# Kernel tuning notes

Measured on AMD Instinct MI355X. Metric: run time of the kernel, lower is better.

Reference implementation:

```python
import jax, jax.numpy as jnp
import numpy as np

B, Q, DIM, HEADS, HEAD_DIM, KV = 32, 4, 2048, 16, 128, 8192


def setup_inputs() -> dict:
    key = jax.random.key(0)
    ks = jax.random.split(key, 9)
    s = 0.02
    return {
        'x': jax.random.normal(ks[0], (B, Q, DIM), jnp.float32),
        'attn_bias': jax.random.normal(ks[1], (B, HEADS, Q, KV), jnp.float32),
        'cache_k': jax.random.normal(ks[2], (B, KV, HEAD_DIM), jnp.float32),
        'cache_v': jax.random.normal(ks[3], (B, KV, HEAD_DIM), jnp.float32),
        'wq': jax.random.normal(ks[4], (DIM, HEADS, HEAD_DIM), jnp.float32) * s,
        'bq': jnp.zeros((HEADS, HEAD_DIM), jnp.float32),
        'wk': jax.random.normal(ks[5], (DIM, HEAD_DIM), jnp.float32) * s,
        'bk': jnp.zeros((HEAD_DIM,), jnp.float32),
        'wv': jax.random.normal(ks[6], (DIM, HEAD_DIM), jnp.float32) * s,
        'bv': jnp.zeros((HEAD_DIM,), jnp.float32),
        'wo': jax.random.normal(ks[7], (HEADS, HEAD_DIM, DIM), jnp.float32) * s,
        'bo': jnp.zeros((DIM,), jnp.float32),
    }


def reference(x, attn_bias, cache_k, cache_v, wq, bq, wk, bk, wv, bv, wo, bo):
    q_len = x.shape[1]
    # projections (MQA: shared single-head K/V)
    q = jnp.einsum('bqd,dhe->bqhe', x, wq) + bq          # [B,Q,H,hd]
    k_new = x @ wk + bk                                   # [B,Q,hd]
    v_new = x @ wv + bv
    # rolling KV cache update: shift left by q_len, write new tokens at end
    k = jnp.roll(cache_k, -q_len, axis=1).at[:, -q_len:].set(k_new)  # [B,KV,hd]
    v = jnp.roll(cache_v, -q_len, axis=1).at[:, -q_len:].set(v_new)
    scale = 1.0 / (k.shape[-1] ** 0.5)
    p = jnp.einsum('bqhe,bke->bhqk', q, k) * scale        # [B,H,Q,KV]
    a = jax.nn.softmax(p + attn_bias, axis=-1)
    o = jnp.einsum('bhqk,bke->bqhe', a, v)                # [B,Q,H,hd]
    return jnp.einsum('bqhe,hed->bqd', o, wo) + bo        # [B,Q,DIM]
```

## Files before the change

kernel.cpp:

```cpp
#include <hip/hip_runtime.h>
#include <cstddef>
#include <cstdint>

#define BATCH 32
#define QL 4
#define DIM 2048
#define NH 16
#define HD 128
#define KVLEN 8192
#define HQ 64
#define CHUNK 512
#define NCK 16
#define KT 64
#define NT 8

typedef __attribute__((ext_vector_type(8))) short bf16x8;
typedef __attribute__((ext_vector_type(4))) float f32x4;

__device__ __forceinline__ unsigned short cvt_bf16(float f) {
    unsigned int u = __builtin_bit_cast(unsigned int, f);
    u += 0x7fffu + ((u >> 16) & 1u);
    return (unsigned short)(u >> 16);
}
__device__ __forceinline__ unsigned int pack2(float a, float b) {
    return (unsigned int)cvt_bf16(a) | ((unsigned int)cvt_bf16(b) << 16);
}
__device__ __forceinline__ float bf16_to_f32(unsigned short s) {
    unsigned int u = ((unsigned int)s) << 16;
    return __builtin_bit_cast(float, u);
}
__device__ __forceinline__ bf16x8 mk_frag(unsigned int a, unsigned int b,
                                          unsigned int c, unsigned int d) {
    unsigned int t[4] = {a, b, c, d};
    return *(const bf16x8*)t;
}

template<int VARIANT>
__global__ __launch_bounds__(256) void gemm_kernel(
    const float* __restrict__ A,
    const float* __restrict__ w0p, const float* __restrict__ w1p,
    const float* __restrict__ w2p,
    const float* __restrict__ b0p, const float* __restrict__ b1p,
    const float* __restrict__ b2p,
    float* __restrict__ o0, float* __restrict__ o1, float* __restrict__ o2)
{
    const int n0 = blockIdx.x * 64;
    const int m0 = blockIdx.y * 64;
    const int kz = blockIdx.z * 512;
    const int tid = threadIdx.x;
    const int wave = tid >> 6, lane = tid & 63;
    const int l15 = lane & 15, quad = lane >> 4;

    const float* W; const float* Bv; int ldw, nc;
    if (VARIANT == 0) {
        if (n0 >= 2176)      { W = w2p; Bv = b2p; ldw = 128;  nc = n0 - 2176; }
        else if (n0 >= 2048) { W = w1p; Bv = b1p; ldw = 128;  nc = n0 - 2048; }
        else                 { W = w0p; Bv = b0p; ldw = 2048; nc = n0; }
    } else { W = w0p; Bv = b0p; ldw = 2048; nc = n0; }

    __shared__ alignas(16) unsigned short a_s[64][72];
    __shared__ alignas(16) unsigned short w_s[64][68];

    const int wn = tid & 63;
    const int wk0 = (tid >> 6) * 4;

    f32x4 acc[4];
    #pragma unroll
    for (int nt = 0; nt < 4; ++nt) acc[nt] = (f32x4){0.f, 0.f, 0.f, 0.f};

    float4 apre[4];
    float wpre[4][4];

    #pragma unroll
    for (int ii = 0; ii < 4; ++ii) {
        int f = tid + 256 * ii, r = f >> 4, c4 = (f & 15) << 2;
        apre[ii] = *(const float4*)&A[(size_t)(m0 + r) * DIM + kz + c4];
    }
    #pragma unroll
    for (int sub = 0; sub < 4; ++sub) {
        int k0 = kz + wk0 + 16 * sub;
        const float* wp = W + (size_t)k0 * ldw + nc + wn;
        #pragma unroll
        for (int j = 0; j < 4; ++j) wpre[sub][j] = wp[(size_t)j * ldw];
    }

    for (int it = 0; it < 8; ++it) {
        __syncthreads();
        #pragma unroll
        for (int ii = 0; ii < 4; ++ii) {
            int f = tid + 256 * ii, r = f >> 4, c4 = (f & 15) << 2;
            *(uint2*)&a_s[r][c4] =
                make_uint2(pack2(apre[ii].x, apre[ii].y), pack2(apre[ii].z, apre[ii].w));
        }
        #pragma unroll
        for (int sub = 0; sub < 4; ++sub) {
            int k0 = wk0 + 16 * sub;
            *(uint2*)&w_s[wn][k0] =
                make_uint2(pack2(wpre[sub][0], wpre[sub][1]),
                           pack2(wpre[sub][2], wpre[sub][3]));
        }
        __syncthreads();
        if (it + 1 < 8) {
            const int kb = kz + (it + 1) * 64;
            #pragma unroll
            for (int ii = 0; ii < 4; ++ii) {
                int f = tid + 256 * ii, r = f >> 4, c4 = (f & 15) << 2;
                apre[ii] = *(const float4*)&A[(size_t)(m0 + r) * DIM + kb + c4];
            }
            #pragma unroll
            for (int sub = 0; sub < 4; ++sub) {
                int k0 = kb + wk0 + 16 * sub;
                const float* wp = W + (size_t)k0 * ldw + nc + wn;
                #pragma unroll
                for (int j = 0; j < 4; ++j) wpre[sub][j] = wp[(size_t)j * ldw];
            }
        }
        #pragma unroll
        for (int kf = 0; kf < 2; ++kf) {
            bf16x8 af = *(const bf16x8*)&a_s[16 * wave + l15][kf * 32 + quad * 8];
            #pragma unroll
            for (int nt = 0; nt < 4; ++nt) {
                uint2 lo = *(const uint2*)&w_s[nt * 16 + l15][kf * 32 + quad * 8];
                uint2 hi = *(const uint2*)&w_s[nt * 16 + l15][kf * 32 + quad * 8 + 4];
                bf16x8 wf = mk_frag(lo.x, lo.y, hi.x, hi.y);
                acc[nt] = __builtin_amdgcn_mfma_f32_16x16x32_bf16(af, wf, acc[nt], 0, 0, 0);
            }
        }
    }
    const bool addb = (blockIdx.z == 0);
    #pragma unroll
    for (int nt = 0; nt < 4; ++nt)
        #pragma unroll
        for (int reg = 0; reg < 4; ++reg) {
            int row = m0 + 16 * wave + quad * 4 + reg;
            int col = n0 + nt * 16 + l15;
            float s = acc[nt][reg];
            if (VARIANT == 1) {
                atomicAdd(&o0[(size_t)row * DIM + col], s + (addb ? Bv[col] : 0.f));
            } else {
                int b = row >> 2, q = row & 3;
                if (col < 2048) {
                    int h = col >> 7, e = col & 127;
                    atomicAdd(&o0[((size_t)(b * 64 + h * 4 + q)) * 128 + e],
                              s + (addb ? b0p[col] : 0.f));
                } else if (col < 2176) {
                    int e = col - 2048;
                    atomicAdd(&o1[(size_t)row * 128 + e], s + (addb ? b1p[e] : 0.f));
                } else {
                    int e = col - 2176;
                    atomicAdd(&o2[(size_t)row * 128 + e], s + (addb ? b2p[e] : 0.f));
                }
            }
        }
}

__global__ __launch_bounds__(256, 2) void attn_kernel(
    const float* __restrict__ qws, const float* __restrict__ kws,
    const float* __restrict__ vws,
    const float* __restrict__ cachek, const float* __restrict__ cachev,
    const float* __restrict__ abias,
    float* __restrict__ opart, float* __restrict__ lpart)
{
    const int ck = blockIdx.x;
    const int b  = blockIdx.y;
    const int tid = threadIdx.x;
    const int wave = tid >> 6, lane = tid & 63;
    const int l15 = lane & 15, quad = lane >> 4;
    const float scale = 0.08838834764831845f;

    __shared__ alignas(16) unsigned short k_s[KT][136];
    __shared__ alignas(16) unsigned short v_sT[HD][68];
    __shared__ alignas(16) unsigned short p_s[4][16][72];

    bf16x8 qf[4];
    {
        const float* qrow = qws + ((size_t)b * HQ + 16 * wave + l15) * HD;
        #pragma unroll
        for (int kf = 0; kf < 4; ++kf) {
            float4 f0 = *(const float4*)&qrow[kf * 32 + quad * 8];
            float4 f1 = *(const float4*)&qrow[kf * 32 + quad * 8 + 4];
            qf[kf] = mk_frag(pack2(f0.x, f0.y), pack2(f0.z, f0.w),
                             pack2(f1.x, f1.y), pack2(f1.z, f1.w));
        }
    }

    const int kbase0 = ck * CHUNK;
    const int ve = tid & 127;
    const int vkq = (tid >> 7);

    const float* bptr[4];
    #pragma unroll
    for (int reg = 0; reg < 4; ++reg) {
        int hq = 16 * wave + quad * 4 + reg;
        int h = hq >> 2, q = hq & 3;
        bptr[reg] = abias + (((size_t)(b * NH + h)) * QL + q) * KVLEN + kbase0 + l15;
    }

    float4 kpre[8];
    float vpre[8][4];
    float bpre[16];

    #pragma unroll
    for (int i = 0; i < 8; ++i) {
        int f = tid + 256 * i;
        int row = f >> 5, e0 = (f & 31) << 2;
        int kv = kbase0 + row;
        const float* pk = (kv < KVLEN - QL)
            ? cachek + ((size_t)b * KVLEN + kv + QL) * HD + e0
            : kws + ((size_t)b * QL + (kv - (KVLEN - QL))) * HD + e0;
        kpre[i] = *(const float4*)pk;
    }
    #pragma unroll
    for (int i = 0; i < 8; ++i) {
        int kv0 = kbase0 + (vkq + 2 * i) * 4;
        #pragma unroll
        for (int j = 0; j < 4; ++j) {
            int kv = kv0 + j;
            const float* pv = (kv < KVLEN - QL)
                ? cachev + ((size_t)b * KVLEN + kv + QL) * HD + ve
                : vws + ((size_t)b * QL + (kv - (KVLEN - QL))) * HD + ve;
            vpre[i][j] = *pv;
        }
    }
    #pragma unroll
    for (int nt = 0; nt < 4; ++nt)
        #pragma unroll
        for (int reg = 0; reg < 4; ++reg)
            bpre[nt * 4 + reg] = bptr[reg][nt * 16];

    f32x4 oa[8];
    #pragma unroll
    for (int n8 = 0; n8 < 8; ++n8) oa[n8] = (f32x4){0.f, 0.f, 0.f, 0.f};
    float lrow[4] = {0.f, 0.f, 0.f, 0.f};

    for (int t = 0; t < NT; ++t) {
        __syncthreads();
        #pragma unroll
        for (int i = 0; i < 8; ++i) {
            int f = tid + 256 * i;
            int row = f >> 5, e0 = (f & 31) << 2;
            *(uint2*)&k_s[row][e0] =
                make_uint2(pack2(kpre[i].x, kpre[i].y), pack2(kpre[i].z, kpre[i].w));
        }
        #pragma unroll
        for (int i = 0; i < 8; ++i) {
            int kv0 = (vkq + 2 * i) * 4;
            *(uint2*)&v_sT[ve][kv0] =
                make_uint2(pack2(vpre[i][0], vpre[i][1]),
                           pack2(vpre[i][2], vpre[i][3]));
        }
        float bias[16];
        #pragma unroll
        for (int j = 0; j < 16; ++j) bias[j] = bpre[j];
        __syncthreads();
        if (t + 1 < NT) {
            const int tb = kbase0 + (t + 1) * KT;
            #pragma unroll
            for (int i = 0; i < 8; ++i) {
                int f = tid + 256 * i;
                int row = f >> 5, e0 = (f & 31) << 2;
                int kv = tb + row;
                const float* pk = (kv < KVLEN - QL)
                    ? cachek + ((size_t)b * KVLEN + kv + QL) * HD + e0
                    : kws + ((size_t)b * QL + (kv - (KVLEN - QL))) * HD + e0;
                kpre[i] = *(const float4*)pk;
            }
            #pragma unroll
            for (int i = 0; i < 8; ++i) {
                int kv0 = tb + (vkq + 2 * i) * 4;
                #pragma unroll
                for (int j = 0; j < 4; ++j) {
                    int kv = kv0 + j;
                    const float* pv = (kv < KVLEN - QL)
                        ? cachev + ((size_t)b * KVLEN + kv + QL) * HD + ve
                        : vws + ((size_t)b * QL + (kv - (KVLEN - QL))) * HD + ve;
                    vpre[i][j] = *pv;
                }
            }
            #pragma unroll
            for (int nt = 0; nt < 4; ++nt)
                #pragma unroll
                for (int reg = 0; reg < 4; ++reg)
                    bpre[nt * 4 + reg] = bptr[reg][(t + 1) * KT + nt * 16];
        }
        f32x4 sacc[4];
        #pragma unroll
        for (int nt = 0; nt < 4; ++nt) sacc[nt] = (f32x4){0.f, 0.f, 0.f, 0.f};
        __builtin_amdgcn_s_setprio(1);
        #pragma unroll
        for (int kf = 0; kf < 4; ++kf) {
            #pragma unroll
            for (int nt = 0; nt < 4; ++nt) {
                bf16x8 kfb = *(const bf16x8*)&k_s[nt * 16 + l15][kf * 32 + quad * 8];
                sacc[nt] = __builtin_amdgcn_mfma_f32_16x16x32_bf16(qf[kf], kfb, sacc[nt], 0, 0, 0);
            }
        }
        __builtin_amdgcn_s_setprio(0);
        #pragma unroll
        for (int nt = 0; nt < 4; ++nt)
            #pragma unroll
            for (int reg = 0; reg < 4; ++reg) {
                float s = sacc[nt][reg] * scale + bias[nt * 4 + reg];
                float p = __expf(s);
                unsigned short pb = cvt_bf16(p);
                lrow[reg] += bf16_to_f32(pb);
                p_s[wave][quad * 4 + reg][nt * 16 + l15] = pb;
            }
        __builtin_amdgcn_s_setprio(1);
        #pragma unroll
        for (int kfp = 0; kfp < 2; ++kfp) {
            uint2 plo = *(const uint2*)&p_s[wave][l15][kfp * 32 + quad * 8];
            uint2 phi = *(const uint2*)&p_s[wave][l15][kfp * 32 + quad * 8 + 4];
            bf16x8 pf = mk_frag(plo.x, plo.y, phi.x, phi.y);
            #pragma unroll
            for (int n8 = 0; n8 < 8; ++n8) {
                uint2 vlo = *(const uint2*)&v_sT[n8 * 16 + l15][kfp * 32 + quad * 8];
                uint2 vhi = *(const uint2*)&v_sT[n8 * 16 + l15][kfp * 32 + quad * 8 + 4];
                bf16x8 vf = mk_frag(vlo.x, vlo.y, vhi.x, vhi.y);
                oa[n8] = __builtin_amdgcn_mfma_f32_16x16x32_bf16(pf, vf, oa[n8], 0, 0, 0);
            }
        }
        __builtin_amdgcn_s_setprio(0);
    }
    #pragma unroll
    for (int reg = 0; reg < 4; ++reg) {
        float v = lrow[reg];
        v += __shfl_xor(v, 1);
        v += __shfl_xor(v, 2);
        v += __shfl_xor(v, 4);
        v += __shfl_xor(v, 8);
        lrow[reg] = v;
    }
    const size_t obase = ((size_t)(b * NCK + ck)) * HQ * HD;
    #pragma unroll
    for (int n8 = 0; n8 < 8; ++n8)
        #pragma unroll
        for (int reg = 0; reg < 4; ++reg) {
            int hq = 16 * wave + quad * 4 + reg;
            int e = n8 * 16 + l15;
            opart[obase + (size_t)hq * HD + e] = oa[n8][reg];
        }
    if (l15 == 0) {
        #pragma unroll
        for (int reg = 0; reg < 4; ++reg) {
            int hq = 16 * wave + quad * 4 + reg;
            lpart[(size_t)(b * NCK + ck) * HQ + hq] = lrow[reg];
        }
    }
}

__global__ __launch_bounds__(128) void combine_kernel(
    const float* __restrict__ opart, const float* __restrict__ lpart,
    float* __restrict__ ored, float* __restrict__ outz)
{
    const int bh = blockIdx.x;
    const int b = bh >> 6, hq = bh & 63;
    const int e = threadIdx.x;
    outz[(size_t)bh * 128 + e] = 0.f;
    float lt = 0.f, ov = 0.f;
    #pragma unroll
    for (int c = 0; c < NCK; ++c) {
        lt += lpart[(b * NCK + c) * HQ + hq];
        ov += opart[((size_t)(b * NCK + c) * HQ + hq) * HD + e];
    }
    int h = hq >> 2, q = hq & 3;
    ored[(size_t)(b * QL + q) * DIM + h * HD + e] = ov / lt;
}

extern "C" void kernel_launch(void* const* d_in, const int* in_sizes, int n_in,
                              void* d_out, int out_size, void* d_ws, size_t ws_size,
                              hipStream_t stream)
{
    const float* x   = (const float*)d_in[0];
    const float* ab  = (const float*)d_in[1];
    const float* cK  = (const float*)d_in[2];
    const float* cV  = (const float*)d_in[3];
    const float* wq  = (const float*)d_in[4];
    const float* bq  = (const float*)d_in[5];
    const float* wk  = (const float*)d_in[6];
    const float* bk  = (const float*)d_in[7];
    const float* wv  = (const float*)d_in[8];
    const float* bv  = (const float*)d_in[9];
    const float* wo  = (const float*)d_in[10];
    const float* bo  = (const float*)d_in[11];
    float* out = (float*)d_out;

    float* ws   = (float*)d_ws;
    float* wsq  = ws;
    float* wsk  = wsq + 262144;
    float* wsv  = wsk + 16384;
    float* wsop = wsv + 16384;
    float* wsl  = wsop + 4194304;
    float* wsor = wsl + 32768;

    hipMemsetAsync(ws, 0, (size_t)(262144 + 16384 + 16384) * sizeof(float),
                   stream);

    gemm_kernel<0><<<dim3(36, 2, 4), 256, 0, stream>>>(
        x, wq, wk, wv, bq, bk, bv, wsq, wsk, wsv);
    attn_kernel<<<dim3(NCK, BATCH), 256, 0, stream>>>(
        wsq, wsk, wsv, cK, cV, ab, wsop, wsl);
    combine_kernel<<<BATCH * HQ, 128, 0, stream>>>(wsop, wsl, wsor, out);
    gemm_kernel<1><<<dim3(32, 2, 4), 256, 0, stream>>>(
        wsor, wo, nullptr, nullptr, bo, nullptr, nullptr, out, nullptr, nullptr);
}
```

Baseline: 397.3 us.

## Remove combine kernel via atomic split-KV accumulation and fused normalization in output GEMM

The attention kernel now accumulates its partial outputs and row sums directly into a per-batch buffer with atomics, instead of writing per-chunk partials that a separate combine kernel reduced. The 1/l normalization and the head-layout transpose move into the A-load of the output-projection GEMM, and zeroing of the output moves into the first GEMM. The KV chunk is halved so the attention grid has twice as many blocks. This removes one kernel launch and the large partial-output round trip through memory, at the cost of atomic contention across chunks and float results that are not bit-for-bit deterministic.

```diff
diff --git a/kernel.cpp b/kernel.cpp
--- a/kernel.cpp
+++ b/kernel.cpp
@@ -9,10 +9,10 @@
 #define HD 128
 #define KVLEN 8192
 #define HQ 64
-#define CHUNK 512
-#define NCK 16
+#define CHUNK 256
+#define NCKB 32
 #define KT 64
-#define NT 8
+#define NT 4
 
 typedef __attribute__((ext_vector_type(8))) short bf16x8;
 typedef __attribute__((ext_vector_type(4))) float f32x4;
@@ -42,7 +42,8 @@
     const float* __restrict__ w2p,
     const float* __restrict__ b0p, const float* __restrict__ b1p,
     const float* __restrict__ b2p,
-    float* __restrict__ o0, float* __restrict__ o1, float* __restrict__ o2)
+    float* __restrict__ o0, float* __restrict__ o1, float* __restrict__ o2,
+    float* __restrict__ zout)
 {
     const int n0 = blockIdx.x * 64;
     const int m0 = blockIdx.y * 64;
@@ -51,12 +52,23 @@
     const int wave = tid >> 6, lane = tid & 63;
     const int l15 = lane & 15, quad = lane >> 4;
 
+    if (VARIANT == 0) {
+        int gbid = (blockIdx.z * 2 + blockIdx.y) * 36 + blockIdx.x;
+        int base = gbid * 256 + tid;
+        #pragma unroll
+        for (int i = 0; i < 4; ++i) {
+            int idx = base + 73728 * i;
+            if (idx < 262144) zout[idx] = 0.f;
+        }
+    }
+
     const float* W; const float* Bv; int ldw, nc;
     if (VARIANT == 0) {
         if (n0 >= 2176)      { W = w2p; Bv = b2p; ldw = 128;  nc = n0 - 2176; }
         else if (n0 >= 2048) { W = w1p; Bv = b1p; ldw = 128;  nc = n0 - 2048; }
         else                 { W = w0p; Bv = b0p; ldw = 2048; nc = n0; }
     } else { W = w0p; Bv = b0p; ldw = 2048; nc = n0; }
+    const float* Lp = w1p;
 
     __shared__ alignas(16) unsigned short a_s[64][72];
     __shared__ alignas(16) unsigned short w_s[64][68];
@@ -74,7 +86,16 @@
     #pragma unroll
     for (int ii = 0; ii < 4; ++ii) {
         int f = tid + 256 * ii, r = f >> 4, c4 = (f & 15) << 2;
-        apre[ii] = *(const float4*)&A[(size_t)(m0 + r) * DIM + kz + c4];
+        int row = m0 + r, cc = kz + c4;
+        if (VARIANT == 1) {
+            int bb = row >> 2, q = row & 3, h = cc >> 7, e0 = cc & 127;
+            int hq = h * 4 + q;
+            float4 v = *(const float4*)&A[((size_t)(bb * 64 + hq)) * 128 + e0];
+            float linv = 1.0f / Lp[bb * 64 + hq];
+            apre[ii] = make_float4(v.x * linv, v.y * linv, v.z * linv, v.w * linv);
+        } else {
+            apre[ii] = *(const float4*)&A[(size_t)row * DIM + cc];
+        }
     }
     #pragma unroll
     for (int sub = 0; sub < 4; ++sub) {
@@ -105,7 +126,16 @@
             #pragma unroll
             for (int ii = 0; ii < 4; ++ii) {
                 int f = tid + 256 * ii, r = f >> 4, c4 = (f & 15) << 2;
-                apre[ii] = *(const float4*)&A[(size_t)(m0 + r) * DIM + kb + c4];
+                int row = m0 + r, cc = kb + c4;
+                if (VARIANT == 1) {
+                    int bb = row >> 2, q = row & 3, h = cc >> 7, e0 = cc & 127;
+                    int hq = h * 4 + q;
+                    float4 v = *(const float4*)&A[((size_t)(bb * 64 + hq)) * 128 + e0];
+                    float linv = 1.0f / Lp[bb * 64 + hq];
+                    apre[ii] = make_float4(v.x * linv, v.y * linv, v.z * linv, v.w * linv);
+                } else {
+                    apre[ii] = *(const float4*)&A[(size_t)row * DIM + cc];
+                }
             }
             #pragma unroll
             for (int sub = 0; sub < 4; ++sub) {
@@ -159,7 +189,7 @@
     const float* __restrict__ vws,
     const float* __restrict__ cachek, const float* __restrict__ cachev,
     const float* __restrict__ abias,
-    float* __restrict__ opart, float* __restrict__ lpart)
+    float* __restrict__ oacc, float* __restrict__ lacc)
 {
     const int ck = blockIdx.x;
     const int b  = blockIdx.y;
@@ -331,40 +361,22 @@
         v += __shfl_xor(v, 8);
         lrow[reg] = v;
     }
-    const size_t obase = ((size_t)(b * NCK + ck)) * HQ * HD;
+    const size_t abase = (size_t)b * HQ * HD;
     #pragma unroll
     for (int n8 = 0; n8 < 8; ++n8)
         #pragma unroll
         for (int reg = 0; reg < 4; ++reg) {
             int hq = 16 * wave + quad * 4 + reg;
             int e = n8 * 16 + l15;
-            opart[obase + (size_t)hq * HD + e] = oa[n8][reg];
+            atomicAdd(&oacc[abase + (size_t)hq * HD + e], oa[n8][reg]);
         }
     if (l15 == 0) {
         #pragma unroll
         for (int reg = 0; reg < 4; ++reg) {
             int hq = 16 * wave + quad * 4 + reg;
-            lpart[(size_t)(b * NCK + ck) * HQ + hq] = lrow[reg];
-        }
-    }
-}
-
-__global__ __launch_bounds__(128) void combine_kernel(
-    const float* __restrict__ opart, const float* __restrict__ lpart,
-    float* __restrict__ ored, float* __restrict__ outz)
-{
-    const int bh = blockIdx.x;
-    const int b = bh >> 6, hq = bh & 63;
-    const int e = threadIdx.x;
-    outz[(size_t)bh * 128 + e] = 0.f;
-    float lt = 0.f, ov = 0.f;
-    #pragma unroll
-    for (int c = 0; c < NCK; ++c) {
-        lt += lpart[(b * NCK + c) * HQ + hq];
-        ov += opart[((size_t)(b * NCK + c) * HQ + hq) * HD + e];
-    }
-    int h = hq >> 2, q = hq & 3;
-    ored[(size_t)(b * QL + q) * DIM + h * HD + e] = ov / lt;
+            atomicAdd(&lacc[b * HQ + hq], lrow[reg]);
+        }
+    }
 }
 
 extern "C" void kernel_launch(void* const* d_in, const int* in_sizes, int n_in,
@@ -389,18 +401,18 @@
     float* wsq  = ws;
     float* wsk  = wsq + 262144;
     float* wsv  = wsk + 16384;
-    float* wsop = wsv + 16384;
-    float* wsl  = wsop + 4194304;
-    float* wsor = wsl + 32768;
-
-    hipMemsetAsync(ws, 0, (size_t)(262144 + 16384 + 16384) * sizeof(float),
-                   stream);
+    float* oacc = wsv + 16384;
+    float* lacc = oacc + 262144;
+
+    hipMemsetAsync(ws, 0,
+        (size_t)(262144 + 16384 + 16384 + 262144 + 2048) * sizeof(float),
+        stream);
 
     gemm_kernel<0><<<dim3(36, 2, 4), 256, 0, stream>>>(
-        x, wq, wk, wv, bq, bk, bv, wsq, wsk, wsv);
-    attn_kernel<<<dim3(NCK, BATCH), 256, 0, stream>>>(
-        wsq, wsk, wsv, cK, cV, ab, wsop, wsl);
-    combine_kernel<<<BATCH * HQ, 128, 0, stream>>>(wsop, wsl, wsor, out);
+        x, wq, wk, wv, bq, bk, bv, wsq, wsk, wsv, out);
+    attn_kernel<<<dim3(NCKB, BATCH), 256, 0, stream>>>(
+        wsq, wsk, wsv, cK, cV, ab, oacc, lacc);
     gemm_kernel<1><<<dim3(32, 2, 4), 256, 0, stream>>>(
-        wsor, wo, nullptr, nullptr, bo, nullptr, nullptr, out, nullptr, nullptr);
-}
+        oacc, wo, lacc, nullptr, bo, nullptr, nullptr, out, nullptr, nullptr,
+        nullptr);
+}
```

After: 400.6 us. No clear change (+0.8%).
